# Performance work log

Measured on AMD Instinct MI355X. Metric: run time of the kernel, lower is better.

## Reference

```python
import jax, jax.numpy as jnp
import numpy as np

N = 10000        # nodes
E = 160000       # active edges
NS = 128         # scalar (0e) channels per tensor
NV = 64          # vector (1o) channels per tensor
LAT = 64         # latent dim
AVG_NEIGH = 16.0
SQ2 = float(np.sqrt(2.0))
SQ3 = float(np.sqrt(3.0))
EPS = 1e-5


def setup_inputs() -> dict:
    key = jax.random.key(0)
    ks = jax.random.split(key, 24)
    rn = lambda k, s: jax.random.normal(k, s, jnp.float32)
    d = {}
    d["latents"] = rn(ks[0], (E, LAT))
    d["node_features"] = rn(ks[1], (N, NS + 3 * NV))
    d["edge_features"] = rn(ks[2], (E, NS + 3 * NV))
    d["edge_sh"] = rn(ks[3], (E, 4))
    d["edge_index"] = jax.random.randint(ks[4], (2, E), 0, N)
    d["atom_type"] = jax.random.randint(ks[5], (N,), 0, 10)
    d["active_edges"] = jnp.arange(E)
    # separable layer norm affine params (node and edge)
    d["g_s_n"] = jnp.ones((NS,), jnp.float32); d["b_s_n"] = jnp.zeros((NS,), jnp.float32)
    d["g_v_n"] = jnp.ones((NV,), jnp.float32)
    d["g_s_e"] = jnp.ones((NS,), jnp.float32); d["b_s_e"] = jnp.zeros((NS,), jnp.float32)
    d["g_v_e"] = jnp.ones((NV,), jnp.float32)
    # FullyConnectedTensorProduct weights (path-normalized init).
    # tp input: 2*NS scalars, 2*NV vectors; sh: 1 scalar + 1 vector;
    # tp output: NS+NV scalars (scalars+gates), NV vectors.
    nSt, nVt, nSo = 2 * NS, 2 * NV, NS + NV
    d["W_ss0"] = rn(ks[6], (nSt, nSo)) / np.sqrt(nSt * 2)
    d["W_vv0"] = rn(ks[7], (nVt, nSo)) / np.sqrt(nVt * 2)
    d["W_sv1"] = rn(ks[8], (nSt, NV)) / np.sqrt(nSt * 3)
    d["W_vs1"] = rn(ks[9], (nVt, NV)) / np.sqrt(nVt * 3)
    d["W_vv1"] = rn(ks[10], (nVt, NV)) / np.sqrt(nVt * 3)
    # lin_post (per-l channel mixing)
    d["Wp_s"] = rn(ks[11], (NS, NS)) / np.sqrt(NS)
    d["Wp_v"] = rn(ks[12], (NV, NV)) / np.sqrt(NV)
    # env_embed_mlps: single linear latent -> weight_numel (NS+NV channels)
    d["W_env"] = rn(ks[13], (LAT, NS + NV)) / np.sqrt(LAT)
    # linear_res
    d["Wr_s"] = rn(ks[14], (NS, NS)) / np.sqrt(NS)
    d["Wr_v"] = rn(ks[15], (NV, NV)) / np.sqrt(NV)
    return d


def _sep_ln(x, g_s, b_s, g_v):
    # separable layer norm: standard LN on scalars, RMS-of-norms on vectors
    s = x[:, :NS]
    v = x[:, NS:].reshape(-1, NV, 3)
    mu = s.mean(-1, keepdims=True)
    var = ((s - mu) ** 2).mean(-1, keepdims=True)
    s = (s - mu) * jax.lax.rsqrt(var + EPS) * g_s + b_s
    vn = jnp.mean(jnp.sum(v * v, -1), -1, keepdims=True)  # (B,1)
    v = v * jax.lax.rsqrt(vn + EPS)[:, :, None] * g_v[None, :, None]
    return s, v


def _forward(latents, node_features, edge_features, edge_sh, edge_index,
             atom_type, active_edges,
             g_s_n, b_s_n, g_v_n, g_s_e, b_s_e, g_v_e,
             W_ss0, W_vv0, W_sv1, W_vs1, W_vv1,
             Wp_s, Wp_v, W_env, Wr_s, Wr_v):
    ec = edge_index[0][active_edges]                      # (E,) center nodes
    ns, nv = _sep_ln(node_features, g_s_n, b_s_n, g_v_n)
    es, ev = _sep_ln(edge_features, g_s_e, b_s_e, g_v_e)
    S = jnp.concatenate([ns[ec], es], axis=-1)            # (E, 2*NS)
    V = jnp.concatenate([nv[ec], ev], axis=1)             # (E, 2*NV, 3)
    sh0 = edge_sh[:, :1]                                  # (E,1)
    sh1 = edge_sh[:, 1:]                                  # (E,3)
    # fully-connected tensor product (tp_in x sh -> gate input)
    dotV = jnp.einsum('ecd,ed->ec', V, sh1) / SQ3         # 1x1->0
    out0 = (S * sh0) @ W_ss0 + dotV @ W_vv0               # (E, NS+NV) scalars
    out_v = (S @ W_sv1)[:, :, None] * sh1[:, None, :]     # 0x1->1
    out_v = out_v + jnp.einsum('ecd,cf->efd', V, W_vs1) * sh0[:, :, None]  # 1x0->1
    cross = jnp.cross(V, sh1[:, None, :]) / SQ2           # 1x1->1
    out_v = out_v + jnp.einsum('ecd,cf->efd', cross, W_vv1)  # (E, NV, 3)
    # gate
    s = jax.nn.silu(out0[:, :NS])
    gates = jax.nn.sigmoid(out0[:, NS:])
    v = out_v * gates[:, :, None]
    # lin_post
    s = s @ Wp_s
    v = jnp.einsum('ecd,cf->efd', v, Wp_v)
    # env weights from latents (elementwise linear per channel)
    w = latents[active_edges] @ W_env                     # (E, NS+NV)
    s = s * w[:, :NS]
    v = v * w[:, NS:][:, :, None]
    msg = jnp.concatenate([s, v.reshape(-1, 3 * NV)], axis=-1)  # (E, 320)
    agg = jax.ops.segment_sum(msg, ec, num_segments=N)
    agg = agg * jnp.float32(1.0 / np.sqrt(AVG_NEIGH))
    # residual linear on raw node features
    rs = node_features[:, :NS] @ Wr_s
    rv = jnp.einsum('ncd,cf->nfd', node_features[:, NS:].reshape(-1, NV, 3), Wr_v)
    res = jnp.concatenate([rs, rv.reshape(-1, 3 * NV)], axis=-1)
    return res + agg


def reference(latents, node_features, edge_features, edge_sh, edge_index,
              atom_type, active_edges,
              g_s_n, b_s_n, g_v_n, g_s_e, b_s_e, g_v_e,
              W_ss0, W_vv0, W_sv1, W_vs1, W_vv1,
              Wp_s, Wp_v, W_env, Wr_s, Wr_v):
    return _forward(latents, node_features, edge_features, edge_sh, edge_index,
                    atom_type, active_edges,
                    g_s_n, b_s_n, g_v_n, g_s_e, b_s_e, g_v_e,
                    W_ss0, W_vv0, W_sv1, W_vs1, W_vv1,
                    Wp_s, Wp_v, W_env, Wr_s, Wr_v)
```

## Files before the change

### kernel.cpp

```cpp
#include <hip/hip_runtime.h>

#define N_NODES 10000
#define N_EDGES 160000
#define NSC 128
#define ROW 320
#define EPS_LN 1e-5f
#define INV_SQ2 0.70710678118654752440f
#define INV_SQ3 0.57735026918962576451f

typedef unsigned short bfraw;
typedef __attribute__((ext_vector_type(8))) short short8;
typedef __attribute__((ext_vector_type(4))) float float4x;

__device__ __forceinline__ float bf2f(bfraw u) {
    union { unsigned int i; float f; } x; x.i = ((unsigned int)u) << 16; return x.f;
}
__device__ __forceinline__ bfraw f2bf(float f) {
    union { float f; unsigned int i; } x; x.f = f;
    unsigned int i = x.i;
    unsigned int lsb = (i >> 16) & 1u;
    i += 0x7fffu + lsb;
    return (bfraw)(i >> 16);
}
template<bool B> __device__ __forceinline__ float LD(const void* p, size_t i) {
    if (B) return bf2f(((const bfraw*)p)[i]);
    else   return ((const float*)p)[i];
}
template<bool B> __device__ __forceinline__ void ST(void* p, size_t i, float v) {
    if (B) ((bfraw*)p)[i] = f2bf(v);
    else   ((float*)p)[i] = v;
}
__device__ __forceinline__ float wred64(float v) {
#pragma unroll
    for (int o = 32; o > 0; o >>= 1) v += __shfl_xor(v, o, 64);
    return v;
}
__device__ __forceinline__ float silu_f(float x) { return x / (1.0f + __expf(-x)); }
__device__ __forceinline__ float sigm_f(float x) { return 1.0f / (1.0f + __expf(-x)); }

#define MFMA16(a, b, c) __builtin_amdgcn_mfma_f32_16x16x32_bf16((a), (b), (c), 0, 0, 0)

__global__ void detect_k(const void* g, int* flag) {
    if (threadIdx.x == 0 && blockIdx.x == 0)
        *flag = (((const unsigned int*)g)[0] == 0x3F803F80u) ? 1 : 0;
}

__global__ void pack_all_k(
    const void* Wss0, const void* Wvv0, const void* Wsv1, const void* Wvs1,
    const void* Wvv1, const void* Wps,  const void* Wpv,  const void* Wenv,
    const void* Wrs,  const void* Wrv,
    bfraw* __restrict__ dst, const int* __restrict__ flag)
{
    int idx = blockIdx.x * 256 + threadIdx.x;
    if (idx >= 159744) return;
    const void* src; int K, N, base;
    if      (idx <  49152) { src = Wss0; K = 256; N = 192; base = 0; }
    else if (idx <  73728) { src = Wvv0; K = 128; N = 192; base = 49152; }
    else if (idx <  90112) { src = Wsv1; K = 256; N =  64; base = 73728; }
    else if (idx <  98304) { src = Wvs1; K = 128; N =  64; base = 90112; }
    else if (idx < 106496) { src = Wvv1; K = 128; N =  64; base = 98304; }
    else if (idx < 122880) { src = Wps;  K = 128; N = 128; base = 106496; }
    else if (idx < 126976) { src = Wpv;  K =  64; N =  64; base = 122880; }
    else if (idx < 139264) { src = Wenv; K =  64; N = 192; base = 126976; }
    else if (idx < 155648) { src = Wrs;  K = 128; N = 128; base = 139264; }
    else                   { src = Wrv;  K =  64; N =  64; base = 155648; }
    int li = idx - base;
    int j = li & 7, l = (li >> 3) & 63, t = li >> 9;
    int NT = N >> 4;
    int nt = t % NT, kt = t / NT;
    int k = kt * 32 + ((l >> 4) << 3) + j;
    int n = (nt << 4) + (l & 15);
    float v = (*flag) ? bf2f(((const bfraw*)src)[(size_t)k * N + n])
                      : ((const float*)src)[(size_t)k * N + n];
    dst[idx] = f2bf(v);
}

template<bool B>
__device__ __forceinline__ void node_ln_body(int n, int lane,
    const void* nf, const void* g_s, const void* b_s, const void* g_v,
    float* __restrict__ nsnv)
{
    size_t base = (size_t)n * ROW;
    float s0 = LD<B>(nf, base + lane), s1 = LD<B>(nf, base + 64 + lane);
    float mu = wred64(s0 + s1) * (1.0f / 128.0f);
    float d0 = s0 - mu, d1 = s1 - mu;
    float var = wred64(d0 * d0 + d1 * d1) * (1.0f / 128.0f);
    float rs = rsqrtf(var + EPS_LN);
    float o0 = d0 * rs * LD<B>(g_s, lane) + LD<B>(b_s, lane);
    float o1 = d1 * rs * LD<B>(g_s, 64 + lane) + LD<B>(b_s, 64 + lane);
    float vx = LD<B>(nf, base + NSC + 3 * lane);
    float vy = LD<B>(nf, base + NSC + 3 * lane + 1);
    float vz = LD<B>(nf, base + NSC + 3 * lane + 2);
    float vn = wred64(vx * vx + vy * vy + vz * vz) * (1.0f / 64.0f);
    float rv = rsqrtf(vn + EPS_LN) * LD<B>(g_v, lane);
    float* o = nsnv + base;
    o[lane] = o0; o[64 + lane] = o1;
    o[NSC + 3 * lane] = vx * rv; o[NSC + 3 * lane + 1] = vy * rv; o[NSC + 3 * lane + 2] = vz * rv;
}

__global__ __launch_bounds__(256) void node_ln_k(
    const void* nf, const void* g_s, const void* b_s, const void* g_v,
    float* __restrict__ nsnv, const int* __restrict__ flag)
{
    int w = threadIdx.x >> 6, lane = threadIdx.x & 63;
    int n = blockIdx.x * 4 + w;
    if (*flag) node_ln_body<true >(n, lane, nf, g_s, b_s, g_v, nsnv);
    else       node_ln_body<false>(n, lane, nf, g_s, b_s, g_v, nsnv);
}

template<bool B>
__device__ void edge_body(char* smem, int tid,
    const float* __restrict__ nsnv,
    const void* ef, const void* esh,
    const int* __restrict__ eidx, const int* __restrict__ act,
    const void* lat,
    const void* g_s_e, const void* b_s_e, const void* g_v_e,
    const bfraw* __restrict__ pk,
    float* __restrict__ agg)
{
    bfraw* SD_u  = (bfraw*)(smem);
    bfraw* V_u   = (bfraw*)(smem + 12544);
    bfraw* sp_u  = (bfraw*)(smem + 25600);
    bfraw* lat_u = (bfraw*)(smem + 29952);
    bfraw* gate_u= (bfraw*)(smem + 32256);
    bfraw* sv_u  = (bfraw*)(smem + 34304);
    float* sh_f  = (float*)(smem + 36352);
    int*   cn_i  = (int*)  (smem + 36608);
    float* wenv_f= (float*)(smem);

    const bfraw* pWss0 = pk;
    const bfraw* pWvv0 = pk + 49152;
    const bfraw* pWsv1 = pk + 73728;
    const bfraw* pWvs1 = pk + 90112;
    const bfraw* pWvv1 = pk + 98304;
    const bfraw* pWps  = pk + 106496;
    const bfraw* pWpv  = pk + 122880;
    const bfraw* pWenv = pk + 126976;

    const int w = tid >> 6, lane = tid & 63;
    const int nl = lane & 15, mq = lane >> 4;
    const int e0 = blockIdx.x * 16;

    for (int i = 0; i < 4; i++) {
        int el = w * 4 + i;
        int e = e0 + el;
        int ae = act[e];
        int cnv = eidx[ae];
        float sh0 = LD<B>(esh, (size_t)e * 4 + 0);
        float b0 = LD<B>(esh, (size_t)e * 4 + 1);
        float b1 = LD<B>(esh, (size_t)e * 4 + 2);
        float b2 = LD<B>(esh, (size_t)e * 4 + 3);

        size_t eb = (size_t)e * ROW;
        float es0 = LD<B>(ef, eb + lane), es1 = LD<B>(ef, eb + 64 + lane);
        float mu = wred64(es0 + es1) * (1.0f / 128.0f);
        float d0 = es0 - mu, d1 = es1 - mu;
        float var = wred64(d0 * d0 + d1 * d1) * (1.0f / 128.0f);
        float rs = rsqrtf(var + EPS_LN);
        es0 = d0 * rs * LD<B>(g_s_e, lane) + LD<B>(b_s_e, lane);
        es1 = d1 * rs * LD<B>(g_s_e, 64 + lane) + LD<B>(b_s_e, 64 + lane);
        float ex = LD<B>(ef, eb + NSC + 3 * lane);
        float ey = LD<B>(ef, eb + NSC + 3 * lane + 1);
        float ez = LD<B>(ef, eb + NSC + 3 * lane + 2);
        float vn = wred64(ex * ex + ey * ey + ez * ez) * (1.0f / 64.0f);
        float rv = rsqrtf(vn + EPS_LN) * LD<B>(g_v_e, lane);
        ex *= rv; ey *= rv; ez *= rv;

        const float* nr = nsnv + (size_t)cnv * ROW;
        float n0 = nr[lane], n1 = nr[64 + lane];
        float nx = nr[NSC + 3 * lane], ny = nr[NSC + 3 * lane + 1], nz = nr[NSC + 3 * lane + 2];

        SD_u[el * 392 + lane]       = f2bf(n0);
        SD_u[el * 392 + 64 + lane]  = f2bf(n1);
        SD_u[el * 392 + 128 + lane] = f2bf(es0);
        SD_u[el * 392 + 192 + lane] = f2bf(es1);
        SD_u[el * 392 + 256 + lane] = f2bf((nx * b0 + ny * b1 + nz * b2) * INV_SQ3);
        SD_u[el * 392 + 320 + lane] = f2bf((ex * b0 + ey * b1 + ez * b2) * INV_SQ3);
        V_u[(el) * 136 + lane]      = f2bf(nx);
        V_u[(16 + el) * 136 + lane] = f2bf(ny);
        V_u[(32 + el) * 136 + lane] = f2bf(nz);
        V_u[(el) * 136 + 64 + lane]      = f2bf(ex);
        V_u[(16 + el) * 136 + 64 + lane] = f2bf(ey);
        V_u[(32 + el) * 136 + 64 + lane] = f2bf(ez);
        lat_u[el * 72 + lane] = f2bf(LD<B>(lat, (size_t)ae * 64 + lane));
        if (lane == 0) {
            sh_f[el * 4] = sh0; sh_f[el * 4 + 1] = b0; sh_f[el * 4 + 2] = b1; sh_f[el * 4 + 3] = b2;
            cn_i[el] = cnv;
        }
    }
    __syncthreads();

    {
        float4x sA[3] = {{0,0,0,0},{0,0,0,0},{0,0,0,0}};
        float4x dA[3] = {{0,0,0,0},{0,0,0,0},{0,0,0,0}};
#pragma unroll
        for (int kt = 0; kt < 8; kt++) {
            short8 a = *(const short8*)&SD_u[nl * 392 + kt * 32 + mq * 8];
#pragma unroll
            for (int t = 0; t < 3; t++) {
                short8 b = *(const short8*)&pWss0[((kt * 12 + 3 * w + t) * 64 + lane) * 8];
                sA[t] = MFMA16(a, b, sA[t]);
            }
        }
#pragma unroll
        for (int kt = 0; kt < 4; kt++) {
            short8 a = *(const short8*)&SD_u[nl * 392 + 256 + kt * 32 + mq * 8];
#pragma unroll
            for (int t = 0; t < 3; t++) {
                short8 b = *(const short8*)&pWvv0[((kt * 12 + 3 * w + t) * 64 + lane) * 8];
                dA[t] = MFMA16(a, b, dA[t]);
            }
        }
#pragma unroll
        for (int t = 0; t < 3; t++) {
            int j = (3 * w + t) * 16 + nl;
#pragma unroll
            for (int r = 0; r < 4; r++) {
                int el = mq * 4 + r;
                float o = sh_f[el * 4] * sA[t][r] + dA[t][r];
                if (j < 128) sp_u[el * 136 + j] = f2bf(silu_f(o));
                else         gate_u[el * 64 + j - 128] = f2bf(sigm_f(o));
            }
        }
    }
    {
        float4x c = {0,0,0,0};
#pragma unroll
        for (int kt = 0; kt < 8; kt++) {
            short8 a = *(const short8*)&SD_u[nl * 392 + kt * 32 + mq * 8];
            short8 b = *(const short8*)&pWsv1[((kt * 4 + w) * 64 + lane) * 8];
            c = MFMA16(a, b, c);
        }
#pragma unroll
        for (int r = 0; r < 4; r++)
            sv_u[(mq * 4 + r) * 64 + w * 16 + nl] = f2bf(c[r]);
    }
    float4x H[3] = {{0,0,0,0},{0,0,0,0},{0,0,0,0}};
    float4x K[3] = {{0,0,0,0},{0,0,0,0},{0,0,0,0}};
#pragma unroll
    for (int d = 0; d < 3; d++) {
#pragma unroll
        for (int kt = 0; kt < 4; kt++) {
            short8 a = *(const short8*)&V_u[(d * 16 + nl) * 136 + kt * 32 + mq * 8];
            short8 bH = *(const short8*)&pWvs1[((kt * 4 + w) * 64 + lane) * 8];
            short8 bK = *(const short8*)&pWvv1[((kt * 4 + w) * 64 + lane) * 8];
            H[d] = MFMA16(a, bH, H[d]);
            K[d] = MFMA16(a, bK, K[d]);
        }
    }
    __syncthreads();

    {
        int f = w * 16 + nl;
#pragma unroll
        for (int r = 0; r < 4; r++) {
            int el = mq * 4 + r;
            float g   = bf2f(gate_u[el * 64 + f]);
            float svv = bf2f(sv_u[el * 64 + f]);
            float s0v = sh_f[el * 4], b0 = sh_f[el * 4 + 1], b1 = sh_f[el * 4 + 2], b2 = sh_f[el * 4 + 3];
            float ov0 = svv * b0 + s0v * H[0][r] + (b2 * K[1][r] - b1 * K[2][r]) * INV_SQ2;
            float ov1 = svv * b1 + s0v * H[1][r] + (b0 * K[2][r] - b2 * K[0][r]) * INV_SQ2;
            float ov2 = svv * b2 + s0v * H[2][r] + (b1 * K[0][r] - b0 * K[1][r]) * INV_SQ2;
            V_u[(el) * 136 + f]      = f2bf(ov0 * g);
            V_u[(16 + el) * 136 + f] = f2bf(ov1 * g);
            V_u[(32 + el) * 136 + f] = f2bf(ov2 * g);
        }
    }
    __syncthreads();

    float4x s2[2] = {{0,0,0,0},{0,0,0,0}};
#pragma unroll
    for (int kt = 0; kt < 4; kt++) {
        short8 a = *(const short8*)&sp_u[nl * 136 + kt * 32 + mq * 8];
#pragma unroll
        for (int t = 0; t < 2; t++) {
            short8 b = *(const short8*)&pWps[((kt * 8 + w + 4 * t) * 64 + lane) * 8];
            s2[t] = MFMA16(a, b, s2[t]);
        }
    }
    float4x v2[3] = {{0,0,0,0},{0,0,0,0},{0,0,0,0}};
#pragma unroll
    for (int d = 0; d < 3; d++) {
#pragma unroll
        for (int kt = 0; kt < 2; kt++) {
            short8 a = *(const short8*)&V_u[(d * 16 + nl) * 136 + kt * 32 + mq * 8];
            short8 b = *(const short8*)&pWpv[((kt * 4 + w) * 64 + lane) * 8];
            v2[d] = MFMA16(a, b, v2[d]);
        }
    }
    float4x wv[3] = {{0,0,0,0},{0,0,0,0},{0,0,0,0}};
#pragma unroll
    for (int kt = 0; kt < 2; kt++) {
        short8 a = *(const short8*)&lat_u[nl * 72 + kt * 32 + mq * 8];
#pragma unroll
        for (int t = 0; t < 3; t++) {
            short8 b = *(const short8*)&pWenv[((kt * 12 + 3 * w + t) * 64 + lane) * 8];
            wv[t] = MFMA16(a, b, wv[t]);
        }
    }
#pragma unroll
    for (int t = 0; t < 3; t++)
#pragma unroll
        for (int r = 0; r < 4; r++)
            wenv_f[(mq * 4 + r) * 192 + (3 * w + t) * 16 + nl] = wv[t][r];
    __syncthreads();

#pragma unroll
    for (int t = 0; t < 2; t++) {
        int c = (w + 4 * t) * 16 + nl;
#pragma unroll
        for (int r = 0; r < 4; r++) {
            int el = mq * 4 + r;
            unsafeAtomicAdd(agg + (size_t)cn_i[el] * ROW + c, s2[t][r] * wenv_f[el * 192 + c]);
        }
    }
    {
        int f = w * 16 + nl;
#pragma unroll
        for (int r = 0; r < 4; r++) {
            int el = mq * 4 + r;
            float we = wenv_f[el * 192 + 128 + f];
            size_t base = (size_t)cn_i[el] * ROW + NSC + 3 * f;
            unsafeAtomicAdd(agg + base,     v2[0][r] * we);
            unsafeAtomicAdd(agg + base + 1, v2[1][r] * we);
            unsafeAtomicAdd(agg + base + 2, v2[2][r] * we);
        }
    }
}

__global__ __launch_bounds__(256, 4) void edge_mfma_k(
    const float* __restrict__ nsnv,
    const void* ef, const void* esh,
    const int* __restrict__ eidx, const int* __restrict__ act,
    const void* lat,
    const void* g_s_e, const void* b_s_e, const void* g_v_e,
    const bfraw* __restrict__ pk,
    float* __restrict__ agg, const int* __restrict__ flag)
{
    __shared__ __align__(16) char smem[36672];
    if (*flag) edge_body<true >(smem, threadIdx.x, nsnv, ef, esh, eidx, act, lat,
        g_s_e, b_s_e, g_v_e, pk, agg);
    else       edge_body<false>(smem, threadIdx.x, nsnv, ef, esh, eidx, act, lat,
        g_s_e, b_s_e, g_v_e, pk, agg);
}

template<bool B>
__device__ void final_body(char* smem, int tid,
    const void* nf, const float* __restrict__ agg,
    const bfraw* __restrict__ pk, void* out)
{
    bfraw* Sn_u = (bfraw*)(smem);
    bfraw* Vn_u = (bfraw*)(smem + 8704);
    const bfraw* pWrs = pk + 139264;
    const bfraw* pWrv = pk + 155648;

    const int w = tid >> 6, lane = tid & 63;
    const int nl = lane & 15, mq = lane >> 4;
    const int n0b = blockIdx.x * 32;

    for (int i = 0; i < 8; i++) {
        int el = w * 8 + i;
        int n = n0b + el;
        bool ok = n < N_NODES;
        size_t base = (size_t)n * ROW;
        float a0 = ok ? LD<B>(nf, base + lane) : 0.0f;
        float a1 = ok ? LD<B>(nf, base + 64 + lane) : 0.0f;
        float vx = ok ? LD<B>(nf, base + NSC + 3 * lane) : 0.0f;
        float vy = ok ? LD<B>(nf, base + NSC + 3 * lane + 1) : 0.0f;
        float vz = ok ? LD<B>(nf, base + NSC + 3 * lane + 2) : 0.0f;
        Sn_u[el * 136 + lane]      = f2bf(a0);
        Sn_u[el * 136 + 64 + lane] = f2bf(a1);
        Vn_u[(el) * 72 + lane]      = f2bf(vx);
        Vn_u[(32 + el) * 72 + lane] = f2bf(vy);
        Vn_u[(64 + el) * 72 + lane] = f2bf(vz);
    }
    __syncthreads();

    {
        const int mt = w & 1, ntb = (w >> 1) * 4;
        float4x c[4] = {{0,0,0,0},{0,0,0,0},{0,0,0,0},{0,0,0,0}};
#pragma unroll
        for (int kt = 0; kt < 4; kt++) {
            short8 a = *(const short8*)&Sn_u[(mt * 16 + nl) * 136 + kt * 32 + mq * 8];
#pragma unroll
            for (int t = 0; t < 4; t++) {
                short8 b = *(const short8*)&pWrs[((kt * 8 + ntb + t) * 64 + lane) * 8];
                c[t] = MFMA16(a, b, c[t]);
            }
        }
#pragma unroll
        for (int t = 0; t < 4; t++) {
            int cc = (ntb + t) * 16 + nl;
#pragma unroll
            for (int r = 0; r < 4; r++) {
                int n = n0b + mt * 16 + mq * 4 + r;
                if (n < N_NODES) {
                    size_t o = (size_t)n * ROW + cc;
                    ST<B>(out, o, c[t][r] + 0.25f * agg[o]);
                }
            }
        }
    }
    {
        float4x c[3][2] = {{{0,0,0,0},{0,0,0,0}},{{0,0,0,0},{0,0,0,0}},{{0,0,0,0},{0,0,0,0}}};
#pragma unroll
        for (int d = 0; d < 3; d++)
#pragma unroll
            for (int h = 0; h < 2; h++)
#pragma unroll
                for (int kt = 0; kt < 2; kt++) {
                    short8 a = *(const short8*)&Vn_u[(d * 32 + h * 16 + nl) * 72 + kt * 32 + mq * 8];
                    short8 b = *(const short8*)&pWrv[((kt * 4 + w) * 64 + lane) * 8];
                    c[d][h] = MFMA16(a, b, c[d][h]);
                }
        int f = w * 16 + nl;
#pragma unroll
        for (int h = 0; h < 2; h++)
#pragma unroll
            for (int r = 0; r < 4; r++) {
                int n = n0b + h * 16 + mq * 4 + r;
                if (n < N_NODES) {
                    size_t o = (size_t)n * ROW + NSC + 3 * f;
                    ST<B>(out, o,     c[0][h][r] + 0.25f * agg[o]);
                    ST<B>(out, o + 1, c[1][h][r] + 0.25f * agg[o + 1]);
                    ST<B>(out, o + 2, c[2][h][r] + 0.25f * agg[o + 2]);
                }
            }
    }
}

__global__ __launch_bounds__(256) void final_mfma_k(
    const void* nf, const float* __restrict__ agg,
    const bfraw* __restrict__ pk, void* out, const int* __restrict__ flag)
{
    __shared__ __align__(16) char smem[22528];
    if (*flag) final_body<true >(smem, threadIdx.x, nf, agg, pk, out);
    else       final_body<false>(smem, threadIdx.x, nf, agg, pk, out);
}

extern "C" void kernel_launch(void* const* d_in, const int* in_sizes, int n_in,
                              void* d_out, int out_size, void* d_ws, size_t ws_size,
                              hipStream_t stream)
{
    const void* latents = d_in[0];
    const void* node_f  = d_in[1];
    const void* edge_f  = d_in[2];
    const void* edge_sh = d_in[3];
    const int* edge_index = (const int*)d_in[4];
    const int* active     = (const int*)d_in[6];
    const void* g_s_n = d_in[7];
    const void* b_s_n = d_in[8];
    const void* g_v_n = d_in[9];
    const void* g_s_e = d_in[10];
    const void* b_s_e = d_in[11];
    const void* g_v_e = d_in[12];

    int*   flag = (int*)d_ws;
    float* agg  = (float*)d_ws + 64;
    float* nsnv = agg + (size_t)N_NODES * ROW;
    bfraw* pk   = (bfraw*)(nsnv + (size_t)N_NODES * ROW);

    detect_k<<<1, 64, 0, stream>>>(g_s_n, flag);
    hipMemsetAsync(agg, 0, (size_t)N_NODES * ROW * sizeof(float), stream);
    pack_all_k<<<624, 256, 0, stream>>>(d_in[13], d_in[14], d_in[15], d_in[16],
        d_in[17], d_in[18], d_in[19], d_in[20], d_in[21], d_in[22], pk, flag);
    node_ln_k<<<N_NODES / 4, 256, 0, stream>>>(node_f, g_s_n, b_s_n, g_v_n, nsnv, flag);
    edge_mfma_k<<<N_EDGES / 16, 256, 0, stream>>>(nsnv, edge_f, edge_sh, edge_index, active,
        latents, g_s_e, b_s_e, g_v_e, pk, agg, flag);
    final_mfma_k<<<(N_NODES + 31) / 32, 256, 0, stream>>>(node_f, agg, pk, (void*)d_out, flag);
}
```

Measured before the change: 713.0 us.

## Replace atomic scatter-add with CSR-sorted gather of bf16 edge messages

The edge kernel no longer does float atomic adds into the node aggregate. It writes per-edge messages in bf16 to a buffer. Three new kernels (count, single-block scan, fill) build a CSR index of edges grouped by destination node, and a gather kernel sums each node's messages without atomics. This removes atomic contention on the aggregate, but adds several extra launches, a 100MB bf16 message round-trip, a serial scan, and rounds messages to bf16 before summing. The cursor buffer is not zeroed separately; the memset covers 81920 bytes, which appears to span both counts and cursor.

```diff
diff --git a/kernel.cpp b/kernel.cpp
--- a/kernel.cpp
+++ b/kernel.cpp
@@ -75,6 +75,41 @@
     dst[idx] = f2bf(v);
 }
 
+__global__ void count_k(const int* __restrict__ eidx, const int* __restrict__ act,
+                        int* __restrict__ counts) {
+    int e = blockIdx.x * 256 + threadIdx.x;
+    if (e < N_EDGES) atomicAdd(&counts[eidx[act[e]]], 1);
+}
+
+__global__ void scan_k(const int* __restrict__ counts, int* __restrict__ starts) {
+    __shared__ int part[256];
+    int t = threadIdx.x;
+    int lo = t * 40, hi = lo + 40 > N_NODES ? N_NODES : lo + 40;
+    int s = 0;
+    for (int i = lo; i < hi; i++) s += counts[i];
+    part[t] = s;
+    __syncthreads();
+    if (t == 0) {
+        int acc = 0;
+        for (int i = 0; i < 256; i++) { int v = part[i]; part[i] = acc; acc += v; }
+        starts[N_NODES] = acc;
+    }
+    __syncthreads();
+    int acc = part[t];
+    for (int i = lo; i < hi; i++) { starts[i] = acc; acc += counts[i]; }
+}
+
+__global__ void fill_k(const int* __restrict__ eidx, const int* __restrict__ act,
+                       const int* __restrict__ starts, int* __restrict__ cursor,
+                       int* __restrict__ csr) {
+    int e = blockIdx.x * 256 + threadIdx.x;
+    if (e < N_EDGES) {
+        int n = eidx[act[e]];
+        int pos = atomicAdd(&cursor[n], 1);
+        csr[starts[n] + pos] = e;
+    }
+}
+
 template<bool B>
 __device__ __forceinline__ void node_ln_body(int n, int lane,
     const void* nf, const void* g_s, const void* b_s, const void* g_v,
@@ -116,7 +151,7 @@
     const void* lat,
     const void* g_s_e, const void* b_s_e, const void* g_v_e,
     const bfraw* __restrict__ pk,
-    float* __restrict__ agg)
+    bfraw* __restrict__ msg)
 {
     bfraw* SD_u  = (bfraw*)(smem);
     bfraw* V_u   = (bfraw*)(smem + 12544);
@@ -125,7 +160,6 @@
     bfraw* gate_u= (bfraw*)(smem + 32256);
     bfraw* sv_u  = (bfraw*)(smem + 34304);
     float* sh_f  = (float*)(smem + 36352);
-    int*   cn_i  = (int*)  (smem + 36608);
     float* wenv_f= (float*)(smem);
 
     const bfraw* pWss0 = pk;
@@ -185,7 +219,6 @@
         lat_u[el * 72 + lane] = f2bf(LD<B>(lat, (size_t)ae * 64 + lane));
         if (lane == 0) {
             sh_f[el * 4] = sh0; sh_f[el * 4 + 1] = b0; sh_f[el * 4 + 2] = b1; sh_f[el * 4 + 3] = b2;
-            cn_i[el] = cnv;
         }
     }
     __syncthreads();
@@ -311,7 +344,7 @@
 #pragma unroll
         for (int r = 0; r < 4; r++) {
             int el = mq * 4 + r;
-            unsafeAtomicAdd(agg + (size_t)cn_i[el] * ROW + c, s2[t][r] * wenv_f[el * 192 + c]);
+            msg[(size_t)(e0 + el) * 320 + c] = f2bf(s2[t][r] * wenv_f[el * 192 + c]);
         }
     }
     {
@@ -320,10 +353,10 @@
         for (int r = 0; r < 4; r++) {
             int el = mq * 4 + r;
             float we = wenv_f[el * 192 + 128 + f];
-            size_t base = (size_t)cn_i[el] * ROW + NSC + 3 * f;
-            unsafeAtomicAdd(agg + base,     v2[0][r] * we);
-            unsafeAtomicAdd(agg + base + 1, v2[1][r] * we);
-            unsafeAtomicAdd(agg + base + 2, v2[2][r] * we);
+            size_t base = (size_t)(e0 + el) * 320 + NSC + 3 * f;
+            msg[base]     = f2bf(v2[0][r] * we);
+            msg[base + 1] = f2bf(v2[1][r] * we);
+            msg[base + 2] = f2bf(v2[2][r] * we);
         }
     }
 }
@@ -335,13 +368,34 @@
     const void* lat,
     const void* g_s_e, const void* b_s_e, const void* g_v_e,
     const bfraw* __restrict__ pk,
-    float* __restrict__ agg, const int* __restrict__ flag)
+    bfraw* __restrict__ msg, const int* __restrict__ flag)
 {
     __shared__ __align__(16) char smem[36672];
     if (*flag) edge_body<true >(smem, threadIdx.x, nsnv, ef, esh, eidx, act, lat,
-        g_s_e, b_s_e, g_v_e, pk, agg);
+        g_s_e, b_s_e, g_v_e, pk, msg);
     else       edge_body<false>(smem, threadIdx.x, nsnv, ef, esh, eidx, act, lat,
-        g_s_e, b_s_e, g_v_e, pk, agg);
+        g_s_e, b_s_e, g_v_e, pk, msg);
+}
+
+__global__ __launch_bounds__(256) void gather_k(
+    const bfraw* __restrict__ msg, const int* __restrict__ starts,
+    const int* __restrict__ csr, float* __restrict__ agg)
+{
+    int w = threadIdx.x >> 6, lane = threadIdx.x & 63;
+    int n = blockIdx.x * 4 + w;
+    if (n >= N_NODES) return;
+    int s0 = starts[n], s1 = starts[n + 1];
+    float a0 = 0, a1 = 0, a2 = 0, a3 = 0, a4 = 0;
+    for (int i = s0; i < s1; i++) {
+        const bfraw* r = msg + (size_t)csr[i] * 320;
+        a0 += bf2f(r[lane]);
+        a1 += bf2f(r[64 + lane]);
+        a2 += bf2f(r[128 + lane]);
+        a3 += bf2f(r[192 + lane]);
+        a4 += bf2f(r[256 + lane]);
+    }
+    float* o = agg + (size_t)n * ROW;
+    o[lane] = a0; o[64 + lane] = a1; o[128 + lane] = a2; o[192 + lane] = a3; o[256 + lane] = a4;
 }
 
 template<bool B>
@@ -455,17 +509,27 @@
     const void* b_s_e = d_in[11];
     const void* g_v_e = d_in[12];
 
-    int*   flag = (int*)d_ws;
-    float* agg  = (float*)d_ws + 64;
-    float* nsnv = agg + (size_t)N_NODES * ROW;
-    bfraw* pk   = (bfraw*)(nsnv + (size_t)N_NODES * ROW);
+    char* ws = (char*)d_ws;
+    int*   flag   = (int*)ws;
+    float* agg    = (float*)(ws + 256);
+    float* nsnv   = (float*)(ws + 12800256);
+    bfraw* pk     = (bfraw*)(ws + 25600256);
+    int*   counts = (int*)(ws + 25919744);
+    int*   cursor = (int*)(ws + 25960704);
+    int*   starts = (int*)(ws + 26001664);
+    int*   csr    = (int*)(ws + 26042624);
+    bfraw* msg    = (bfraw*)(ws + 26682624);
 
     detect_k<<<1, 64, 0, stream>>>(g_s_n, flag);
-    hipMemsetAsync(agg, 0, (size_t)N_NODES * ROW * sizeof(float), stream);
+    hipMemsetAsync(counts, 0, 81920, stream);
     pack_all_k<<<624, 256, 0, stream>>>(d_in[13], d_in[14], d_in[15], d_in[16],
         d_in[17], d_in[18], d_in[19], d_in[20], d_in[21], d_in[22], pk, flag);
+    count_k<<<625, 256, 0, stream>>>(edge_index, active, counts);
+    scan_k<<<1, 256, 0, stream>>>(counts, starts);
+    fill_k<<<625, 256, 0, stream>>>(edge_index, active, starts, cursor, csr);
     node_ln_k<<<N_NODES / 4, 256, 0, stream>>>(node_f, g_s_n, b_s_n, g_v_n, nsnv, flag);
     edge_mfma_k<<<N_EDGES / 16, 256, 0, stream>>>(nsnv, edge_f, edge_sh, edge_index, active,
-        latents, g_s_e, b_s_e, g_v_e, pk, agg, flag);
+        latents, g_s_e, b_s_e, g_v_e, pk, msg, flag);
+    gather_k<<<N_NODES / 4, 256, 0, stream>>>(msg, starts, csr, agg);
     final_mfma_k<<<(N_NODES + 31) / 32, 256, 0, stream>>>(node_f, agg, pk, (void*)d_out, flag);
 }
```

After: 606.0 us. 1.18x faster.
